# Kernel tuning notes

Hardware: AMD Instinct MI355X
Metric: run time of the kernel (lower is better)

Reference implementation:

```python
import jax, jax.numpy as jnp
import numpy as np

B, S, D, H, HD, FF, L = 16384, 5, 6, 2, 3, 2048, 4
EPS = 1e-5


def setup_inputs() -> dict:
    key = jax.random.key(0)
    ks = jax.random.split(key, 20)
    s = lambda fan: 1.0 / np.sqrt(fan)
    inp = {
        'x': jax.random.normal(ks[0], (B, S, D), dtype=jnp.float32),
        # per-layer stacked MHA params (in_proj split into q/k/v) and out_proj
        'Wq': jax.random.uniform(ks[1], (L, D, D), jnp.float32, -s(D), s(D)),
        'bq': jax.random.uniform(ks[2], (L, D), jnp.float32, -s(D), s(D)),
        'Wk': jax.random.uniform(ks[3], (L, D, D), jnp.float32, -s(D), s(D)),
        'bk': jax.random.uniform(ks[4], (L, D), jnp.float32, -s(D), s(D)),
        'Wv': jax.random.uniform(ks[5], (L, D, D), jnp.float32, -s(D), s(D)),
        'bv': jax.random.uniform(ks[6], (L, D), jnp.float32, -s(D), s(D)),
        'Wo': jax.random.uniform(ks[7], (L, D, D), jnp.float32, -s(D), s(D)),
        'bo': jax.random.uniform(ks[8], (L, D), jnp.float32, -s(D), s(D)),
        # FFN: linear1 D->FF, linear2 FF->D (torch Linear stores [out,in])
        'W1': jax.random.uniform(ks[9], (L, FF, D), jnp.float32, -s(D), s(D)),
        'b1': jax.random.uniform(ks[10], (L, FF), jnp.float32, -s(D), s(D)),
        'W2': jax.random.uniform(ks[11], (L, D, FF), jnp.float32, -s(FF), s(FF)),
        'b2': jax.random.uniform(ks[12], (L, D), jnp.float32, -s(FF), s(FF)),
        # layernorms
        'g1': jnp.ones((L, D), jnp.float32),
        'be1': jnp.zeros((L, D), jnp.float32),
        'g2': jnp.ones((L, D), jnp.float32),
        'be2': jnp.zeros((L, D), jnp.float32),
        # classification head Linear(30, 2)
        'Wfc': jax.random.uniform(ks[13], (2, S * D), jnp.float32, -s(S * D), s(S * D)),
        'bfc': jax.random.uniform(ks[14], (2,), jnp.float32, -s(S * D), s(S * D)),
    }
    return inp


def _layernorm(x, g, b):
    m = jnp.mean(x, axis=-1, keepdims=True)
    v = jnp.mean(jnp.square(x - m), axis=-1, keepdims=True)
    return (x - m) * jax.lax.rsqrt(v + EPS) * g + b


def _encoder_stack(x, Wq, bq, Wk, bk, Wv, bv, Wo, bo, W1, b1, W2, b2, g1, be1, g2, be2):
    scale = 1.0 / np.sqrt(HD)
    for i in range(L):  # small fixed loop over layers
        # multi-head self-attention (post-norm, eval mode: dropout = identity)
        q = (x @ Wq[i].T + bq[i]).reshape(B, S, H, HD)
        k = (x @ Wk[i].T + bk[i]).reshape(B, S, H, HD)
        v = (x @ Wv[i].T + bv[i]).reshape(B, S, H, HD)
        scores = jnp.einsum('bqhd,bkhd->bhqk', q, k) * scale
        attn = jax.nn.softmax(scores, axis=-1)
        ctx = jnp.einsum('bhqk,bkhd->bqhd', attn, v).reshape(B, S, D)
        x = _layernorm(x + ctx @ Wo[i].T + bo[i], g1[i], be1[i])
        # FFN: relu(x W1^T + b1) W2^T + b2
        h = jax.nn.relu(x @ W1[i].T + b1[i])  # [B,S,FF]
        x = _layernorm(x + h @ W2[i].T + b2[i], g2[i], be2[i])
    return x


def reference(x, Wq, bq, Wk, bk, Wv, bv, Wo, bo, W1, b1, W2, b2, g1, be1, g2, be2, Wfc, bfc):
    t = _encoder_stack(x, Wq, bq, Wk, bk, Wv, bv, Wo, bo, W1, b1, W2, b2, g1, be1, g2, be2)
    flat = t.reshape(-1, S * D)
    logits = flat @ Wfc.T + bfc
    return jax.nn.softmax(logits, axis=1)
```

## Files before the change

kernel.cpp:

```cpp
#include <hip/hip_runtime.h>
#include <math.h>

#define NL 4
#define NBATCH 16384
#define NS 5
#define ND 6
#define NH 2
#define NHD 3
#define NFF 2048
#define EPSV 1e-5f

#define ITEMS 32
#define TPB 512
#define NJT 128
#define ROW (NS * ND)
#define NVAL (ITEMS * ROW)

typedef __fp16 v4h __attribute__((ext_vector_type(4)));
typedef __fp16 v2h __attribute__((ext_vector_type(2)));
typedef float f32x4 __attribute__((ext_vector_type(4)));

union HU { uint2 u; v4h h; __fp16 f[4]; };

__device__ inline unsigned pk_u32(float a, float b) {
    union { v2h h; unsigned u; } x;
    x.h = __builtin_amdgcn_cvt_pkrtz(a, b);
    return x.u;
}

__device__ __align__(16) uint4 WPK[NL * NJT * 64];
__device__ __align__(16) f32x4 B1T[NL * NJT * 4];

__global__ void pack_kernel(const float* __restrict__ W1,
                            const float* __restrict__ b1,
                            const float* __restrict__ W2) {
    int idx = blockIdx.x * 256 + threadIdx.x;
    if (idx < NL * NJT * 64) {
        int lane = idx & 63, jt = (idx >> 6) & 127, l = idx >> 13;
        int cc = lane & 15, g = lane >> 4;
        HU o1; o1.u = make_uint2(0u, 0u);
        if (g < 2) {
            int j = jt * 16 + cc;
#pragma unroll
            for (int e = 0; e < 4; ++e) {
                int k = 4 * g + e;
                o1.f[e] = (k < ND) ? (__fp16)W1[(size_t)(l * NFF + j) * ND + k]
                                   : (__fp16)0.f;
            }
        }
        HU o2; o2.u = make_uint2(0u, 0u);
        if (cc < ND) {
#pragma unroll
            for (int e = 0; e < 4; ++e) {
                int j = jt * 16 + 4 * g + e;
                o2.f[e] = (__fp16)W2[(size_t)(l * ND + cc) * NFF + j];
            }
        }
        WPK[idx] = make_uint4(o1.u.x, o1.u.y, o2.u.x, o2.u.y);
    } else if (idx < NL * NJT * 64 + NL * NJT * 4) {
        int t = idx - NL * NJT * 64;
        int g = t & 3, jt = (t >> 2) & 127, l = t >> 9;
        f32x4 v;
        v.x = b1[l * NFF + jt * 16 + 4 * g + 0];
        v.y = b1[l * NFF + jt * 16 + 4 * g + 1];
        v.z = b1[l * NFF + jt * 16 + 4 * g + 2];
        v.w = b1[l * NFF + jt * 16 + 4 * g + 3];
        B1T[t] = v;
    }
}

__global__ __launch_bounds__(TPB, 4) void encoder_kernel(
    const float* __restrict__ xin,
    const float* __restrict__ Wq, const float* __restrict__ bq,
    const float* __restrict__ Wk, const float* __restrict__ bk,
    const float* __restrict__ Wv, const float* __restrict__ bv,
    const float* __restrict__ Wo, const float* __restrict__ bo,
    const float* __restrict__ b2,
    const float* __restrict__ g1, const float* __restrict__ be1,
    const float* __restrict__ g2, const float* __restrict__ be2,
    const float* __restrict__ Wfc, const float* __restrict__ bfc,
    float* __restrict__ out) {
    __shared__ float xs[NVAL];
    __shared__ float kvs[ITEMS * NS * 2 * ND];
    __shared__ float ybuf[4 * 2 * 5 * 64 * 4];

    const int tid = threadIdx.x;
    const int base = blockIdx.x * ITEMS;

    if (tid < NVAL / 4)
        ((float4*)xs)[tid] = ((const float4*)(xin + (size_t)base * ROW))[tid];
    __syncthreads();

    const bool act = tid < ITEMS * NS;
    const int ai = tid / NS;
    const int at = tid - ai * NS;

    const int lane = tid & 63;
    const int w = tid >> 6;
    const int jq = w & 3, ig = w >> 2;
    const int c16 = lane & 15, g = lane >> 4;

    v4h hz; hz.x = hz.y = hz.z = hz.w = (__fp16)0.f;

    for (int l = 0; l < NL; ++l) {
        const uint4* wp = WPK + (size_t)(l * NJT + jq * 32) * 64 + lane;
        const f32x4* b1p = B1T + (size_t)(l * NJT + jq * 32) * 4 + g;
        uint4 wpf[2][4]; f32x4 bpf[2][4];
#pragma unroll
        for (int p = 0; p < 4; ++p) { wpf[0][p] = wp[p * 64]; bpf[0][p] = b1p[p * 4]; }

        float xr[ND], qv[ND];
        if (act) {
#pragma unroll
            for (int d = 0; d < ND; ++d) xr[d] = xs[(ai * NS + at) * ND + d];
#pragma unroll
            for (int d = 0; d < ND; ++d) {
                float aq = bq[l * ND + d], ak = bk[l * ND + d], av = bv[l * ND + d];
#pragma unroll
                for (int e = 0; e < ND; ++e) {
                    aq += Wq[(l * ND + d) * ND + e] * xr[e];
                    ak += Wk[(l * ND + d) * ND + e] * xr[e];
                    av += Wv[(l * ND + d) * ND + e] * xr[e];
                }
                qv[d] = aq;
                kvs[(ai * NS + at) * 2 * ND + d] = ak;
                kvs[(ai * NS + at) * 2 * ND + ND + d] = av;
            }
        }
        __syncthreads();
        if (act) {
            const float scale = 0.57735026919f;
            float ctx[ND];
#pragma unroll
            for (int h = 0; h < NH; ++h) {
                float sc[NS];
                float mx = -1e30f;
#pragma unroll
                for (int u = 0; u < NS; ++u) {
                    float s = 0.f;
#pragma unroll
                    for (int d = 0; d < NHD; ++d)
                        s += qv[h * NHD + d] * kvs[(ai * NS + u) * 2 * ND + h * NHD + d];
                    s *= scale;
                    sc[u] = s;
                    mx = fmaxf(mx, s);
                }
                float sum = 0.f;
#pragma unroll
                for (int u = 0; u < NS; ++u) {
                    sc[u] = __expf(sc[u] - mx);
                    sum += sc[u];
                }
                float inv = 1.f / sum;
#pragma unroll
                for (int d = 0; d < NHD; ++d) {
                    float cx = 0.f;
#pragma unroll
                    for (int u = 0; u < NS; ++u)
                        cx += sc[u] * kvs[(ai * NS + u) * 2 * ND + ND + h * NHD + d];
                    ctx[h * NHD + d] = cx * inv;
                }
            }
            float yr[ND];
#pragma unroll
            for (int d = 0; d < ND; ++d) {
                float a = bo[l * ND + d];
#pragma unroll
                for (int e = 0; e < ND; ++e) a += Wo[(l * ND + d) * ND + e] * ctx[e];
                yr[d] = a + xr[d];
            }
            float m = 0.f;
#pragma unroll
            for (int d = 0; d < ND; ++d) m += yr[d];
            m *= (1.f / ND);
            float va = 0.f;
#pragma unroll
            for (int d = 0; d < ND; ++d) { float dv = yr[d] - m; va += dv * dv; }
            va *= (1.f / ND);
            float r = rsqrtf(va + EPSV);
#pragma unroll
            for (int d = 0; d < ND; ++d)
                xs[(ai * NS + at) * ND + d] =
                    (yr[d] - m) * r * g1[l * ND + d] + be1[l * ND + d];
        }
        __syncthreads();
        v4h xb[5];
#pragma unroll
        for (int mt = 0; mt < 5; ++mt) {
            HU u; u.u = make_uint2(0u, 0u);
            int row = ig * 80 + mt * 16 + c16;
            if (g == 0) {
                float2 a = *(const float2*)&xs[row * 6];
                float2 b = *(const float2*)&xs[row * 6 + 2];
                u.u.x = pk_u32(a.x, a.y);
                u.u.y = pk_u32(b.x, b.y);
            } else if (g == 1) {
                float2 a = *(const float2*)&xs[row * 6 + 4];
                u.u.x = pk_u32(a.x, a.y);
            }
            xb[mt] = u.h;
        }
        f32x4 y0 = {0.f, 0.f, 0.f, 0.f}, y1 = y0, y2 = y0, y3 = y0, y4 = y0;
#pragma unroll
        for (int gq = 0; gq < 8; ++gq) {
            const int cur = gq & 1, nxt = cur ^ 1;
            if (gq < 7) {
#pragma unroll
                for (int p = 0; p < 4; ++p) {
                    wpf[nxt][p] = wp[(gq * 4 + 4 + p) * 64];
                    bpf[nxt][p] = b1p[(gq * 4 + 4 + p) * 4];
                }
            }
#pragma unroll
            for (int p = 0; p < 4; ++p) {
                HU a1; a1.u = make_uint2(wpf[cur][p].x, wpf[cur][p].y);
                HU a2; a2.u = make_uint2(wpf[cur][p].z, wpf[cur][p].w);
                f32x4 bb = bpf[cur][p];
#define FFN_STEP(YREG, XB)                                                      \
                {                                                               \
                    f32x4 hh = __builtin_amdgcn_mfma_f32_16x16x16f16(           \
                        a1.h, (XB), bb, 0, 0, 0);                               \
                    HU hb;                                                      \
                    hb.u.x = pk_u32(hh.x, hh.y);                                \
                    hb.u.y = pk_u32(hh.z, hh.w);                                \
                    hb.h = __builtin_elementwise_max(hb.h, hz);                 \
                    YREG = __builtin_amdgcn_mfma_f32_16x16x16f16(               \
                        a2.h, hb.h, YREG, 0, 0, 0);                             \
                }
                FFN_STEP(y0, xb[0])
                FFN_STEP(y1, xb[1])
                FFN_STEP(y2, xb[2])
                FFN_STEP(y3, xb[3])
                FFN_STEP(y4, xb[4])
#undef FFN_STEP
            }
        }
        {
            f32x4* yb = (f32x4*)ybuf;
            int sb = ((jq * 2 + ig) * 5) * 64 + lane;
            yb[sb + 0 * 64] = y0;
            yb[sb + 1 * 64] = y1;
            yb[sb + 2 * 64] = y2;
            yb[sb + 3 * 64] = y3;
            yb[sb + 4 * 64] = y4;
        }
        __syncthreads();
        if (act) {
            int R = ai * NS + at;
            int igR = R / 80, rm = R % 80;
            int mtR = rm / 16, cR = rm & 15;
            float yr[ND];
#pragma unroll
            for (int d = 0; d < ND; ++d) {
                int gR = d >> 2, iR = d & 3;
                float s = 0.f;
#pragma unroll
                for (int q = 0; q < 4; ++q)
                    s += ybuf[(((q * 2 + igR) * 5 + mtR) * 64 + gR * 16 + cR) * 4 + iR];
                yr[d] = xs[R * ND + d] + s + b2[l * ND + d];
            }
            float m = 0.f;
#pragma unroll
            for (int d = 0; d < ND; ++d) m += yr[d];
            m *= (1.f / ND);
            float va = 0.f;
#pragma unroll
            for (int d = 0; d < ND; ++d) { float dv = yr[d] - m; va += dv * dv; }
            va *= (1.f / ND);
            float r = rsqrtf(va + EPSV);
#pragma unroll
            for (int d = 0; d < ND; ++d)
                xs[R * ND + d] = (yr[d] - m) * r * g2[l * ND + d] + be2[l * ND + d];
        }
        __syncthreads();
    }
    if (tid < ITEMS) {
        float l0 = bfc[0], l1 = bfc[1];
#pragma unroll
        for (int v = 0; v < ROW; ++v) {
            float xv = xs[tid * ROW + v];
            l0 += Wfc[v] * xv;
            l1 += Wfc[ROW + v] * xv;
        }
        float mx = fmaxf(l0, l1);
        float e0 = __expf(l0 - mx), e1 = __expf(l1 - mx);
        float inv = 1.f / (e0 + e1);
        out[(size_t)(base + tid) * 2 + 0] = e0 * inv;
        out[(size_t)(base + tid) * 2 + 1] = e1 * inv;
    }
}

extern "C" void kernel_launch(void* const* d_in, const int* in_sizes, int n_in,
                              void* d_out, int out_size, void* d_ws, size_t ws_size,
                              hipStream_t stream) {
    (void)in_sizes; (void)n_in; (void)d_ws; (void)ws_size; (void)out_size;
    const float* x = (const float*)d_in[0];
    const float* Wq = (const float*)d_in[1];
    const float* bq = (const float*)d_in[2];
    const float* Wk = (const float*)d_in[3];
    const float* bk = (const float*)d_in[4];
    const float* Wv = (const float*)d_in[5];
    const float* bv = (const float*)d_in[6];
    const float* Wo = (const float*)d_in[7];
    const float* bo = (const float*)d_in[8];
    const float* W1 = (const float*)d_in[9];
    const float* b1 = (const float*)d_in[10];
    const float* W2 = (const float*)d_in[11];
    const float* b2 = (const float*)d_in[12];
    const float* g1 = (const float*)d_in[13];
    const float* be1 = (const float*)d_in[14];
    const float* g2 = (const float*)d_in[15];
    const float* be2 = (const float*)d_in[16];
    const float* Wfc = (const float*)d_in[17];
    const float* bfc = (const float*)d_in[18];
    float* out = (float*)d_out;

    const int npack = NL * NJT * 64 + NL * NJT * 4;
    hipLaunchKernelGGL(pack_kernel, dim3((npack + 255) / 256), dim3(256), 0, stream,
                       W1, b1, W2);
    hipLaunchKernelGGL(encoder_kernel, dim3(NBATCH / ITEMS), dim3(TPB), 0, stream,
                       x, Wq, bq, Wk, bk, Wv, bv, Wo, bo, b2, g1, be1, g2, be2,
                       Wfc, bfc, out);
}
```

Measured before the change: 69.63 us.

## Switch FFN to 16x16x32 MFMA with bias folded into the weights

Replaces the pair of 16x16x16 f16 MFMAs per FF tile with 16x16x32 MFMAs that handle two 16-column FF tiles per W2 step. The W1 bias is folded into the packed A operand as a seventh input column, multiplied by a constant 1.0 in the activation vector, which removes the separate bias loads. The repacked weights use three arrays, and the number of MFMA issues on the second GEMM is halved. The cost is that b1 is now rounded to fp16, and the K=32 instruction carries more zero padding.

Measured after the change: 61.68 us. 1.13x faster.

```diff
diff --git a/kernel.cpp b/kernel.cpp
--- a/kernel.cpp
+++ b/kernel.cpp
@@ -12,60 +12,59 @@
 
 #define ITEMS 32
 #define TPB 512
-#define NJT 128
+#define NPAIR 64
 #define ROW (NS * ND)
 #define NVAL (ITEMS * ROW)
 
-typedef __fp16 v4h __attribute__((ext_vector_type(4)));
+typedef __fp16 v8h __attribute__((ext_vector_type(8)));
 typedef __fp16 v2h __attribute__((ext_vector_type(2)));
 typedef float f32x4 __attribute__((ext_vector_type(4)));
 
-union HU { uint2 u; v4h h; __fp16 f[4]; };
+union HU8 { uint4 u; v8h h; __fp16 f[8]; };
 
 __device__ inline unsigned pk_u32(float a, float b) {
     union { v2h h; unsigned u; } x;
     x.h = __builtin_amdgcn_cvt_pkrtz(a, b);
     return x.u;
 }
-
-__device__ __align__(16) uint4 WPK[NL * NJT * 64];
-__device__ __align__(16) f32x4 B1T[NL * NJT * 4];
+__device__ inline unsigned packh(float a, float b) {
+    union { __fp16 h[2]; unsigned u; } x;
+    x.h[0] = (__fp16)a; x.h[1] = (__fp16)b; return x.u;
+}
+
+__device__ __align__(16) uint4 W1A[NL * NPAIR * 64];
+__device__ __align__(16) uint4 W1B[NL * NPAIR * 64];
+__device__ __align__(16) uint4 W2P[NL * NPAIR * 64];
 
 __global__ void pack_kernel(const float* __restrict__ W1,
                             const float* __restrict__ b1,
                             const float* __restrict__ W2) {
+    const int TOT = NL * NPAIR * 64;
     int idx = blockIdx.x * 256 + threadIdx.x;
-    if (idx < NL * NJT * 64) {
-        int lane = idx & 63, jt = (idx >> 6) & 127, l = idx >> 13;
-        int cc = lane & 15, g = lane >> 4;
-        HU o1; o1.u = make_uint2(0u, 0u);
-        if (g < 2) {
-            int j = jt * 16 + cc;
-#pragma unroll
-            for (int e = 0; e < 4; ++e) {
-                int k = 4 * g + e;
-                o1.f[e] = (k < ND) ? (__fp16)W1[(size_t)(l * NFF + j) * ND + k]
-                                   : (__fp16)0.f;
-            }
-        }
-        HU o2; o2.u = make_uint2(0u, 0u);
-        if (cc < ND) {
-#pragma unroll
-            for (int e = 0; e < 4; ++e) {
-                int j = jt * 16 + 4 * g + e;
-                o2.f[e] = (__fp16)W2[(size_t)(l * ND + cc) * NFF + j];
-            }
-        }
-        WPK[idx] = make_uint4(o1.u.x, o1.u.y, o2.u.x, o2.u.y);
-    } else if (idx < NL * NJT * 64 + NL * NJT * 4) {
-        int t = idx - NL * NJT * 64;
-        int g = t & 3, jt = (t >> 2) & 127, l = t >> 9;
-        f32x4 v;
-        v.x = b1[l * NFF + jt * 16 + 4 * g + 0];
-        v.y = b1[l * NFF + jt * 16 + 4 * g + 1];
-        v.z = b1[l * NFF + jt * 16 + 4 * g + 2];
-        v.w = b1[l * NFF + jt * 16 + 4 * g + 3];
-        B1T[t] = v;
+    if (idx >= 3 * TOT) return;
+    int arr = idx / TOT, t = idx - arr * TOT;
+    int lane = t & 63, p = (t >> 6) & 63, l = t >> 12;
+    int r = lane & 15, g = lane >> 4;
+    HU8 o; o.u = make_uint4(0u, 0u, 0u, 0u);
+    if (arr < 2) {
+        if (g == 0) {
+            int j = (2 * p + arr) * 16 + r;
+#pragma unroll
+            for (int e = 0; e < ND; ++e)
+                o.f[e] = (__fp16)W1[(size_t)(l * NFF + j) * ND + e];
+            o.f[6] = (__fp16)b1[l * NFF + j];
+            o.f[7] = (__fp16)0.f;
+        }
+        if (arr == 0) W1A[t] = o.u; else W1B[t] = o.u;
+    } else {
+        if (r < ND) {
+#pragma unroll
+            for (int e = 0; e < 8; ++e) {
+                int j = p * 32 + ((e < 4) ? (4 * g + e) : (16 + 4 * g + e - 4));
+                o.f[e] = (__fp16)W2[(size_t)(l * ND + r) * NFF + j];
+            }
+        }
+        W2P[t] = o.u;
     }
 }
 
@@ -100,14 +99,20 @@
     const int jq = w & 3, ig = w >> 2;
     const int c16 = lane & 15, g = lane >> 4;
 
-    v4h hz; hz.x = hz.y = hz.z = hz.w = (__fp16)0.f;
+    v8h z8; z8 = (v8h)(__fp16)0.f;
+    const f32x4 cz = {0.f, 0.f, 0.f, 0.f};
 
     for (int l = 0; l < NL; ++l) {
-        const uint4* wp = WPK + (size_t)(l * NJT + jq * 32) * 64 + lane;
-        const f32x4* b1p = B1T + (size_t)(l * NJT + jq * 32) * 4 + g;
-        uint4 wpf[2][4]; f32x4 bpf[2][4];
-#pragma unroll
-        for (int p = 0; p < 4; ++p) { wpf[0][p] = wp[p * 64]; bpf[0][p] = b1p[p * 4]; }
+        const uint4* pw1a = W1A + (size_t)(l * NPAIR + jq * 16) * 64 + lane;
+        const uint4* pw1b = W1B + (size_t)(l * NPAIR + jq * 16) * 64 + lane;
+        const uint4* pw2  = W2P + (size_t)(l * NPAIR + jq * 16) * 64 + lane;
+        uint4 wpf[2][6];
+#pragma unroll
+        for (int pp = 0; pp < 2; ++pp) {
+            wpf[0][pp * 3 + 0] = pw1a[pp * 64];
+            wpf[0][pp * 3 + 1] = pw1b[pp * 64];
+            wpf[0][pp * 3 + 2] = pw2[pp * 64];
+        }
 
         float xr[ND], qv[ND];
         if (act) {
@@ -184,48 +189,52 @@
                     (yr[d] - m) * r * g1[l * ND + d] + be1[l * ND + d];
         }
         __syncthreads();
-        v4h xb[5];
+        v8h xb[5];
 #pragma unroll
         for (int mt = 0; mt < 5; ++mt) {
-            HU u; u.u = make_uint2(0u, 0u);
-            int row = ig * 80 + mt * 16 + c16;
+            HU8 u; u.u = make_uint4(0u, 0u, 0u, 0u);
             if (g == 0) {
-                float2 a = *(const float2*)&xs[row * 6];
-                float2 b = *(const float2*)&xs[row * 6 + 2];
-                u.u.x = pk_u32(a.x, a.y);
-                u.u.y = pk_u32(b.x, b.y);
-            } else if (g == 1) {
-                float2 a = *(const float2*)&xs[row * 6 + 4];
-                u.u.x = pk_u32(a.x, a.y);
+                int row = ig * 80 + mt * 16 + c16;
+                const float* xp = &xs[row * 6];
+                u.u.x = pk_u32(xp[0], xp[1]);
+                u.u.y = pk_u32(xp[2], xp[3]);
+                u.u.z = pk_u32(xp[4], xp[5]);
+                u.u.w = 0x00003c00u;
             }
             xb[mt] = u.h;
         }
-        f32x4 y0 = {0.f, 0.f, 0.f, 0.f}, y1 = y0, y2 = y0, y3 = y0, y4 = y0;
+        f32x4 y0 = cz, y1 = cz, y2 = cz, y3 = cz, y4 = cz;
 #pragma unroll
         for (int gq = 0; gq < 8; ++gq) {
             const int cur = gq & 1, nxt = cur ^ 1;
             if (gq < 7) {
 #pragma unroll
-                for (int p = 0; p < 4; ++p) {
-                    wpf[nxt][p] = wp[(gq * 4 + 4 + p) * 64];
-                    bpf[nxt][p] = b1p[(gq * 4 + 4 + p) * 4];
-                }
-            }
-#pragma unroll
-            for (int p = 0; p < 4; ++p) {
-                HU a1; a1.u = make_uint2(wpf[cur][p].x, wpf[cur][p].y);
-                HU a2; a2.u = make_uint2(wpf[cur][p].z, wpf[cur][p].w);
-                f32x4 bb = bpf[cur][p];
+                for (int pp = 0; pp < 2; ++pp) {
+                    int pofs = (gq * 2 + 2 + pp) * 64;
+                    wpf[nxt][pp * 3 + 0] = pw1a[pofs];
+                    wpf[nxt][pp * 3 + 1] = pw1b[pofs];
+                    wpf[nxt][pp * 3 + 2] = pw2[pofs];
+                }
+            }
+#pragma unroll
+            for (int pp = 0; pp < 2; ++pp) {
+                HU8 a1; a1.u = wpf[cur][pp * 3 + 0];
+                HU8 b1f; b1f.u = wpf[cur][pp * 3 + 1];
+                HU8 w2f; w2f.u = wpf[cur][pp * 3 + 2];
 #define FFN_STEP(YREG, XB)                                                      \
                 {                                                               \
-                    f32x4 hh = __builtin_amdgcn_mfma_f32_16x16x16f16(           \
-                        a1.h, (XB), bb, 0, 0, 0);                               \
-                    HU hb;                                                      \
-                    hb.u.x = pk_u32(hh.x, hh.y);                                \
-                    hb.u.y = pk_u32(hh.z, hh.w);                                \
-                    hb.h = __builtin_elementwise_max(hb.h, hz);                 \
-                    YREG = __builtin_amdgcn_mfma_f32_16x16x16f16(               \
-                        a2.h, hb.h, YREG, 0, 0, 0);                             \
+                    f32x4 h0 = __builtin_amdgcn_mfma_f32_16x16x32_f16(          \
+                        a1.h, (XB), cz, 0, 0, 0);                               \
+                    f32x4 h1 = __builtin_amdgcn_mfma_f32_16x16x32_f16(          \
+                        b1f.h, (XB), cz, 0, 0, 0);                              \
+                    HU8 hb;                                                     \
+                    hb.u.x = pk_u32(h0.x, h0.y);                                \
+                    hb.u.y = pk_u32(h0.z, h0.w);                                \
+                    hb.u.z = pk_u32(h1.x, h1.y);                                \
+                    hb.u.w = pk_u32(h1.z, h1.w);                                \
+                    hb.h = __builtin_elementwise_max(hb.h, z8);                 \
+                    YREG = __builtin_amdgcn_mfma_f32_16x16x32_f16(              \
+                        w2f.h, hb.h, YREG, 0, 0, 0);                            \
                 }
                 FFN_STEP(y0, xb[0])
                 FFN_STEP(y1, xb[1])
@@ -315,7 +324,7 @@
     const float* bfc = (const float*)d_in[18];
     float* out = (float*)d_out;
 
-    const int npack = NL * NJT * 64 + NL * NJT * 4;
+    const int npack = 3 * NL * NPAIR * 64;
     hipLaunchKernelGGL(pack_kernel, dim3((npack + 255) / 256), dim3(256), 0, stream,
                        W1, b1, W2);
     hipLaunchKernelGGL(encoder_kernel, dim3(NBATCH / ITEMS), dim3(TPB), 0, stream,
```
